# Kernel tuning notes

Hardware: AMD Instinct MI355X
Metric: run time of the kernel (lower is better)

## Reference

```python
import jax, jax.numpy as jnp
import numpy as np

N_NODES = 100000
N_EDGES = 1600000
N_GRAPHS = 512
IN_F, H1, H2 = 128, 128, 256
N_GROUPS, N_FAM = 16, 10


def setup_inputs() -> dict:
    key = jax.random.key(0)
    ks = jax.random.split(key, 8)
    x = jax.random.normal(ks[0], (N_NODES, IN_F), dtype=jnp.float32)
    edge_index = jax.random.randint(ks[1], (2, N_EDGES), 0, N_NODES, dtype=jnp.int64)
    batch = jnp.sort(jax.random.randint(ks[2], (N_NODES,), 0, N_GRAPHS, dtype=jnp.int64))
    W1 = jax.random.normal(ks[3], (IN_F, H1), dtype=jnp.float32) / np.sqrt(IN_F)
    b1 = jnp.zeros((H1,), dtype=jnp.float32)
    W2 = jax.random.normal(ks[4], (H1, H2), dtype=jnp.float32) / np.sqrt(H1)
    b2 = jnp.zeros((H2,), dtype=jnp.float32)
    Wg = jax.random.normal(ks[5], (H2, N_GROUPS), dtype=jnp.float32) / np.sqrt(H2)
    bg = jnp.zeros((N_GROUPS,), dtype=jnp.float32)
    Wf = jax.random.normal(ks[6], (N_GROUPS, H2, N_FAM), dtype=jnp.float32) / np.sqrt(H2)
    bf = jnp.zeros((N_GROUPS, N_FAM), dtype=jnp.float32)
    return {"x": x, "edge_index": edge_index, "batch": batch,
            "W1": W1, "b1": b1, "W2": W2, "b2": b2,
            "Wg": Wg, "bg": bg, "Wf": Wf, "bf": bf}


def gcn_conv(x, W, b, src, dst, num_nodes):
    # PyG GCNConv: add self-loops, symmetric normalization, scatter-add aggregation.
    xw = x @ W  # [N, out]
    deg = jax.ops.segment_sum(jnp.ones((src.shape[0],), x.dtype), dst,
                              num_segments=num_nodes) + 1.0  # +1 self-loop
    dinv = jax.lax.rsqrt(deg)
    coef = dinv[src] * dinv[dst]            # [E]
    msg = xw[src] * coef[:, None]           # gather + scale (memory-bound)
    agg = jax.ops.segment_sum(msg, dst, num_segments=num_nodes)
    agg = agg + xw * (dinv * dinv)[:, None]  # self-loop contribution
    return agg + b


def reference(x, edge_index, batch, W1, b1, W2, b2, Wg, bg, Wf, bf):
    src, dst = edge_index[0], edge_index[1]
    h = jax.nn.relu(gcn_conv(x, W1, b1, src, dst, N_NODES))
    # dropout p=0.5 is identity in eval mode
    h = gcn_conv(h, W2, b2, src, dst, N_NODES)
    # global mean pool over graphs
    sums = jax.ops.segment_sum(h, batch, num_segments=N_GRAPHS)       # [G, H2]
    cnts = jax.ops.segment_sum(jnp.ones((N_NODES,), h.dtype), batch,
                               num_segments=N_GRAPHS)
    pooled = sums / jnp.maximum(cnts, 1.0)[:, None]
    group_logits = pooled @ Wg + bg                                   # [G, num_groups]
    family_logits = jnp.einsum('bd,gdf->gbf', pooled, Wf) + bf[:, None, :]
    return group_logits, family_logits
```

## Files before the change

### kernel.cpp

```cpp
#include <hip/hip_runtime.h>

#define NN 100000
#define NE 1600000
#define NGR 512
#define KF 128
#define H2F 256
#define NGRP 16
#define NFAM 10

#define CH 128
#define NCHUNK ((NN + CH - 1) / CH)
#define PT 6656
#define NT ((NE + PT - 1) / PT)
#define PREPB_BLKS 64

typedef __attribute__((ext_vector_type(8))) short short8;
typedef __attribute__((ext_vector_type(4))) float floatx4;
typedef __attribute__((ext_vector_type(2))) float floatx2;
typedef __attribute__((ext_vector_type(2))) unsigned uintx2;

__device__ __forceinline__ unsigned short f2bf(float f) {
  unsigned u = __float_as_uint(f);
  unsigned r = (u + 0x7fff + ((u >> 16) & 1)) >> 16;
  return (unsigned short)r;
}
__device__ __forceinline__ float2 bf2f(unsigned u) {
  float2 r;
  r.x = __uint_as_float(u << 16);
  r.y = __uint_as_float(u & 0xffff0000u);
  return r;
}
__device__ __forceinline__ unsigned short pk_fp8(float a, float b) {
  return (unsigned short)__builtin_amdgcn_cvt_pk_fp8_f32(a, b, 0, false);
}
__device__ __forceinline__ floatx2 unpk_fp8(unsigned short u) {
  return __builtin_amdgcn_cvt_pk_f32_fp8((int)u, false);
}


__global__ __launch_bounds__(256) void k_histprep(const int* __restrict__ ei,
                                                  int* __restrict__ tot,
                                                  const float* __restrict__ W,
                                                  unsigned short* __restrict__ Bp) {
  __shared__ int lh[NCHUNK];
  int tid = threadIdx.x;
  if (blockIdx.x >= NT) {
    int idx = (blockIdx.x - NT) * 256 + tid;
    int j = idx & 7;
    int l = (idx >> 3) & 63;
    int rest = idx >> 9;
    int nc = rest & 7;
    int kc = rest >> 3;
    int k = kc * 32 + (l >> 4) * 8 + j;
    int nn = nc * 16 + (l & 15);
    Bp[idx] = f2bf(W[k * KF + nn]);
    return;
  }
  for (int g = tid; g < NCHUNK; g += 256) lh[g] = 0;
  __syncthreads();
  int base = blockIdx.x * PT;
  int nv = min(PT, NE - base);
  for (int i = tid; i < nv; i += 256) atomicAdd(&lh[ei[NE + base + i] >> 7], 1);
  __syncthreads();
  for (int g = tid; g < NCHUNK; g += 256) {
    int v = lh[g];
    if (v) atomicAdd(&tot[g], v);
  }
}


__global__ __launch_bounds__(256) void k_scantot(const int* __restrict__ tot,
                                                 int* __restrict__ cbase,
                                                 int* __restrict__ cursor) {
  __shared__ int ssc[256];
  int tid = threadIdx.x;
  int v4[4]; int loc = 0;
#pragma unroll
  for (int j = 0; j < 4; ++j) {
    int idx = tid * 4 + j;
    v4[j] = (idx < NCHUNK) ? tot[idx] : 0;
    loc += v4[j];
  }
  ssc[tid] = loc;
  __syncthreads();
  for (int off = 1; off < 256; off <<= 1) {
    int val = (tid >= off) ? ssc[tid - off] : 0;
    __syncthreads();
    ssc[tid] += val;
    __syncthreads();
  }
  int excl = ssc[tid] - loc;
#pragma unroll
  for (int j = 0; j < 4; ++j) {
    int idx = tid * 4 + j;
    if (idx < NCHUNK) { cbase[idx] = excl; cursor[idx] = excl; }
    excl += v4[j];
  }
  if (tid == 255) cbase[NCHUNK] = excl;
}


__global__ __launch_bounds__(256) void k_pscatter(const int* __restrict__ ei,
                                                  int* __restrict__ cursor,
                                                  int2* __restrict__ erec) {
  __shared__ int2 stage[PT];
  __shared__ int lstart[NCHUNK];
  __shared__ int lrun[NCHUNK];
  __shared__ int gbase[NCHUNK];
  __shared__ int ssc[256];
  int t0 = blockIdx.x, tid = threadIdx.x;
  for (int g = tid; g < NCHUNK; g += 256) lrun[g] = 0;
  __syncthreads();
  int base = t0 * PT;
  int nv = min(PT, NE - base);
  for (int i = tid; i < nv; i += 256) atomicAdd(&lrun[ei[NE + base + i] >> 7], 1);
  __syncthreads();
  int v4[4]; int loc = 0;
#pragma unroll
  for (int j = 0; j < 4; ++j) {
    int idx = tid * 4 + j;
    v4[j] = (idx < NCHUNK) ? lrun[idx] : 0;
    loc += v4[j];
  }
  ssc[tid] = loc;
  __syncthreads();
  for (int off = 1; off < 256; off <<= 1) {
    int val = (tid >= off) ? ssc[tid - off] : 0;
    __syncthreads();
    ssc[tid] += val;
    __syncthreads();
  }
  int excl = ssc[tid] - loc;
#pragma unroll
  for (int j = 0; j < 4; ++j) {
    int idx = tid * 4 + j;
    if (idx < NCHUNK) lstart[idx] = excl;
    excl += v4[j];
  }
  __syncthreads();
  for (int g = tid; g < NCHUNK; g += 256) {
    int cnt = ((g + 1 < NCHUNK) ? lstart[g + 1] : nv) - lstart[g];
    gbase[g] = cnt ? atomicAdd(&cursor[g], cnt) : 0;
    lrun[g] = lstart[g];
  }
  __syncthreads();
  for (int i = tid; i < nv; i += 256) {
    int s = ei[base + i], d = ei[NE + base + i];
    int pos = atomicAdd(&lrun[d >> 7], 1);
    stage[pos] = make_int2(s, d);
  }
  __syncthreads();
  for (int j = tid; j < nv; j += 256) {
    int2 r = stage[j];
    int g = r.y >> 7;
    erec[gbase[g] + (j - lstart[g])] = r;
  }
}


__global__ __launch_bounds__(256) void k_sort(const int2* __restrict__ erec,
                                              const int* __restrict__ cbase,
                                              int* __restrict__ esrc,
                                              float* __restrict__ ew,
                                              int* __restrict__ rowptr,
                                              float* __restrict__ dinv) {
  __shared__ int hist[CH];
  __shared__ int lrun[CH];
  __shared__ float ldv[CH];
  __shared__ int sc[256];
  const int c = blockIdx.x, tid = threadIdx.x;
  const int e0 = cbase[c], e1 = cbase[c + 1];
  const int nv = e1 - e0;
  if (tid < CH) hist[tid] = 0;
  __syncthreads();
  for (int i = tid; i < nv; i += 256) atomicAdd(&hist[erec[e0 + i].y & (CH - 1)], 1);
  __syncthreads();
  int deg = (tid < CH) ? hist[tid] : 0;
  sc[tid] = deg;
  __syncthreads();
  for (int off = 1; off < 256; off <<= 1) {
    int val = (tid >= off) ? sc[tid - off] : 0;
    __syncthreads();
    sc[tid] += val;
    __syncthreads();
  }
  int excl = sc[tid] - deg;
  int node = c * CH + tid;
  if (tid < CH) {
    lrun[tid] = excl;
    if (node < NN) {
      float dv = rsqrtf((float)(deg + 1));
      rowptr[node] = e0 + excl;
      dinv[node] = dv;
      ldv[tid] = dv;
    } else if (node == NN) {
      rowptr[NN] = e0 + excl;
    }
  }
  __syncthreads();
  for (int i = tid; i < nv; i += 256) {
    int2 r = erec[e0 + i];
    int ln = r.y & (CH - 1);
    int pos = atomicAdd(&lrun[ln], 1);
    esrc[e0 + pos] = r.x;
    ew[e0 + pos] = ldv[ln];
  }
}


__global__ __launch_bounds__(256) void k_gemm_mfma(const float* __restrict__ A,
                                                   const unsigned short* __restrict__ Bp,
                                                   const float* __restrict__ dinv,
                                                   unsigned short* __restrict__ C) {
  constexpr int K = 128;
  constexpr int NCH = KF / 16;
  const int wv = blockIdx.x * 4 + (threadIdx.x >> 6);
  const int row0 = wv * 16;
  if (row0 >= NN) return;
  const int lane = threadIdx.x & 63;
  const int m = lane & 15;
  const int q = lane >> 4;

  floatx4 acc[NCH];
#pragma unroll
  for (int i = 0; i < NCH; ++i) acc[i] = (floatx4){0.f, 0.f, 0.f, 0.f};

  const int arow = row0 + m;
#pragma unroll
  for (int kc = 0; kc < 4; ++kc) {
    const float* ap = A + (size_t)arow * K + kc * 32 + q * 8;
    float4 f0 = *(const float4*)ap;
    float4 f1 = *(const float4*)(ap + 4);
    short8 af;
    af[0] = (short)f2bf(f0.x); af[1] = (short)f2bf(f0.y);
    af[2] = (short)f2bf(f0.z); af[3] = (short)f2bf(f0.w);
    af[4] = (short)f2bf(f1.x); af[5] = (short)f2bf(f1.y);
    af[6] = (short)f2bf(f1.z); af[7] = (short)f2bf(f1.w);
    const unsigned short* bp = Bp + (size_t)kc * NCH * 512;
#pragma unroll
    for (int nc = 0; nc < NCH; ++nc) {
      short8 bfr = *(const short8*)(bp + (size_t)nc * 512 + lane * 8);
      acc[nc] = __builtin_amdgcn_mfma_f32_16x16x32_bf16(af, bfr, acc[nc], 0, 0, 0);
    }
  }

  float ds[4];
#pragma unroll
  for (int r = 0; r < 4; ++r) ds[r] = dinv[row0 + q * 4 + r];
#pragma unroll
  for (int nc = 0; nc < 4; ++nc) {
#pragma unroll
    for (int r = 0; r < 4; ++r) {
      int row = row0 + q * 4 + r;
      C[(size_t)row * 64 + nc * 16 + m] =
          pk_fp8(acc[nc][r] * ds[r], acc[nc + 4][r] * ds[r]);
    }
  }
}


__global__ __launch_bounds__(128) void k_agg1(const unsigned short* __restrict__ p,
                                              const float* __restrict__ bias,
                                              const int* __restrict__ rowptr,
                                              const int* __restrict__ esrc,
                                              const float* __restrict__ dinv,
                                              unsigned short* __restrict__ outp) {
  const int n = blockIdx.x * 2 + (threadIdx.x >> 6);
  const int t = threadIdx.x & 63;
  const int u = t & 31;
  const int half = t >> 5;
  const unsigned* __restrict__ prow = (const unsigned*)p;

  float a0 = 0.f, a1 = 0.f, a2 = 0.f, a3 = 0.f;

  if (half == 0) {
    unsigned v = prow[((unsigned)n << 5) + u];
    floatx2 lo = unpk_fp8((unsigned short)(v & 0xffffu));
    floatx2 hi = unpk_fp8((unsigned short)(v >> 16));
    a0 = lo.x; a1 = lo.y; a2 = hi.x; a3 = hi.y;
  }

  const int r0 = rowptr[n];
  const int r1 = rowptr[n + 1];
  int i = r0;

#define PAIR_TIER(NP)                                                  \
  for (; i + 2 * (NP) <= r1; i += 2 * (NP)) {                          \
    const int ib = i + half;                                           \
    unsigned s[NP];                                                    \
    _Pragma("unroll") for (int j = 0; j < (NP); ++j)                   \
        s[j] = (unsigned)esrc[ib + 2 * j];                             \
    unsigned v[NP];                                                    \
    _Pragma("unroll") for (int j = 0; j < (NP); ++j)                   \
        v[j] = prow[(s[j] << 5) + u];                                  \
    _Pragma("unroll") for (int j = 0; j < (NP); ++j) {                 \
      floatx2 lo = unpk_fp8((unsigned short)(v[j] & 0xffffu));         \
      floatx2 hi = unpk_fp8((unsigned short)(v[j] >> 16));             \
      a0 += lo.x; a1 += lo.y; a2 += hi.x; a3 += hi.y;                  \
    }                                                                  \
  }

  PAIR_TIER(8)
  PAIR_TIER(4)
  PAIR_TIER(2)
  PAIR_TIER(1)
#undef PAIR_TIER

  if (i < r1 && half == 0) {
    unsigned s = (unsigned)esrc[i];
    unsigned v = prow[(s << 5) + u];
    floatx2 lo = unpk_fp8((unsigned short)(v & 0xffffu));
    floatx2 hi = unpk_fp8((unsigned short)(v >> 16));
    a0 += lo.x; a1 += lo.y; a2 += hi.x; a3 += hi.y;
  }

  a0 += __shfl_down(a0, 32, 64);
  a1 += __shfl_down(a1, 32, 64);
  a2 += __shfl_down(a2, 32, 64);
  a3 += __shfl_down(a3, 32, 64);

  if (half == 0) {
    const float dn = dinv[n];
    float2 blo = *(const float2*)(bias + 2 * u);
    float2 bhi = *(const float2*)(bias + 64 + 2 * u);
    float x0 = fmaxf(fmaf(dn, a0, blo.x), 0.f) * dn;
    float x1 = fmaxf(fmaf(dn, a1, bhi.x), 0.f) * dn;
    float x2 = fmaxf(fmaf(dn, a2, blo.y), 0.f) * dn;
    float x3 = fmaxf(fmaf(dn, a3, bhi.y), 0.f) * dn;
    unsigned lo = pk_fp8(x0, x1);
    unsigned hi = pk_fp8(x2, x3);
    ((unsigned*)outp)[((unsigned)n << 5) + u] = lo | (hi << 16);
  }
}


__global__ __launch_bounds__(512) void k_aggpool(const unsigned short* __restrict__ p,
                                                 const int* __restrict__ batch,
                                                 const int* __restrict__ rowptr,
                                                 const int* __restrict__ esrc,
                                                 const float* __restrict__ ew,
                                                 const float* __restrict__ dinv,
                                                 const float* __restrict__ W2,
                                                 const float* __restrict__ b2,
                                                 const float* __restrict__ Wg,
                                                 const float* __restrict__ bg,
                                                 const float* __restrict__ Wf,
                                                 const float* __restrict__ bfb,
                                                 float* __restrict__ out) {
  __shared__ float sacc[8][128];
  __shared__ float pr[KF];
  __shared__ float pp[H2F];
  __shared__ int bnd[2];
  const int g = blockIdx.x;
  const int tid = threadIdx.x;
  if (tid < 2) {
    int target = g + tid;
    int lo = 0, hi = NN;
    while (lo < hi) { int mid = (lo + hi) >> 1; if (batch[mid] < target) lo = mid + 1; else hi = mid; }
    bnd[tid] = lo;
  }
  __syncthreads();
  const int start = bnd[0], end = bnd[1];
  const int wv = tid >> 6, t = tid & 63, u = t & 31, half = t >> 5;
  const unsigned* __restrict__ prow = (const unsigned*)p;

  float a0 = 0.f, a1 = 0.f, a2 = 0.f, a3 = 0.f;

  const int e0 = rowptr[start];
  const int e1 = rowptr[end];

#define EDGE_STEP(idx)                                                 \
  {                                                                    \
    unsigned s_ = (unsigned)esrc[(idx)];                               \
    float w_ = ew[(idx)];                                              \
    unsigned v_ = prow[(s_ << 5) + u];                                 \
    floatx2 lo = unpk_fp8((unsigned short)(v_ & 0xffffu));             \
    floatx2 hi = unpk_fp8((unsigned short)(v_ >> 16));                 \
    a0 = fmaf(w_, lo.x, a0); a1 = fmaf(w_, lo.y, a1);                  \
    a2 = fmaf(w_, hi.x, a2); a3 = fmaf(w_, hi.y, a3);                  \
  }

  int i = e0 + wv * 2 + half;
  for (; i + 48 < e1; i += 64) {
    int i0 = i, i1 = i + 16, i2 = i + 32, i3 = i + 48;
    unsigned s0 = (unsigned)esrc[i0], s1 = (unsigned)esrc[i1];
    unsigned s2 = (unsigned)esrc[i2], s3 = (unsigned)esrc[i3];
    float w0 = ew[i0], w1 = ew[i1], w2 = ew[i2], w3 = ew[i3];
    unsigned v0 = prow[(s0 << 5) + u];
    unsigned v1 = prow[(s1 << 5) + u];
    unsigned v2 = prow[(s2 << 5) + u];
    unsigned v3 = prow[(s3 << 5) + u];
    floatx2 f;
    f = unpk_fp8((unsigned short)(v0 & 0xffffu)); a0 = fmaf(w0, f.x, a0); a1 = fmaf(w0, f.y, a1);
    f = unpk_fp8((unsigned short)(v0 >> 16));     a2 = fmaf(w0, f.x, a2); a3 = fmaf(w0, f.y, a3);
    f = unpk_fp8((unsigned short)(v1 & 0xffffu)); a0 = fmaf(w1, f.x, a0); a1 = fmaf(w1, f.y, a1);
    f = unpk_fp8((unsigned short)(v1 >> 16));     a2 = fmaf(w1, f.x, a2); a3 = fmaf(w1, f.y, a3);
    f = unpk_fp8((unsigned short)(v2 & 0xffffu)); a0 = fmaf(w2, f.x, a0); a1 = fmaf(w2, f.y, a1);
    f = unpk_fp8((unsigned short)(v2 >> 16));     a2 = fmaf(w2, f.x, a2); a3 = fmaf(w2, f.y, a3);
    f = unpk_fp8((unsigned short)(v3 & 0xffffu)); a0 = fmaf(w3, f.x, a0); a1 = fmaf(w3, f.y, a1);
    f = unpk_fp8((unsigned short)(v3 >> 16));     a2 = fmaf(w3, f.x, a2); a3 = fmaf(w3, f.y, a3);
  }
  for (; i < e1; i += 16) EDGE_STEP(i)
#undef EDGE_STEP

  for (int n = start + wv * 2 + half; n < end; n += 16) {
    float w_ = dinv[n];
    unsigned v_ = prow[((unsigned)n << 5) + u];
    floatx2 lo = unpk_fp8((unsigned short)(v_ & 0xffffu));
    floatx2 hi = unpk_fp8((unsigned short)(v_ >> 16));
    a0 = fmaf(w_, lo.x, a0); a1 = fmaf(w_, lo.y, a1);
    a2 = fmaf(w_, hi.x, a2); a3 = fmaf(w_, hi.y, a3);
  }

  a0 += __shfl_down(a0, 32, 64);
  a1 += __shfl_down(a1, 32, 64);
  a2 += __shfl_down(a2, 32, 64);
  a3 += __shfl_down(a3, 32, 64);
  if (half == 0) {
    sacc[wv][2 * u] = a0;
    sacc[wv][2 * u + 1] = a2;
    sacc[wv][2 * u + 64] = a1;
    sacc[wv][2 * u + 65] = a3;
  }
  __syncthreads();
  if (tid < KF) {
    float v = 0.f;
#pragma unroll
    for (int w = 0; w < 8; ++w) v += sacc[w][tid];
    float c = fmaxf((float)(end - start), 1.f);
    pr[tid] = v / c;
  }
  __syncthreads();
  if (tid < H2F) {
    float acc = b2[tid];
#pragma unroll 8
    for (int d = 0; d < KF; ++d) acc = fmaf(pr[d], W2[d * H2F + tid], acc);
    pp[tid] = acc;
  }
  __syncthreads();
  if (tid < NGRP) {
    float a = bg[tid];
    for (int d = 0; d < H2F; ++d) a = fmaf(pp[d], Wg[d * NGRP + tid], a);
    out[g * NGRP + tid] = a;
  } else if (tid >= 64 && tid < 64 + NGRP * NFAM) {
    int uu = tid - 64;
    int gg = uu / NFAM;
    int ff = uu % NFAM;
    float a = bfb[gg * NFAM + ff];
    for (int d = 0; d < H2F; ++d) a = fmaf(pp[d], Wf[(gg * H2F + d) * NFAM + ff], a);
    out[NGR * NGRP + (size_t)gg * NGR * NFAM + g * NFAM + ff] = a;
  }
}


extern "C" void kernel_launch(void* const* d_in, const int* in_sizes, int n_in,
                              void* d_out, int out_size, void* d_ws, size_t ws_size,
                              hipStream_t stream) {
  const float* x    = (const float*)d_in[0];
  const int*   ei   = (const int*)d_in[1];
  const int*   batch= (const int*)d_in[2];
  const float* W1   = (const float*)d_in[3];
  const float* b1   = (const float*)d_in[4];
  const float* W2   = (const float*)d_in[5];
  const float* b2   = (const float*)d_in[6];
  const float* Wg   = (const float*)d_in[7];
  const float* bg   = (const float*)d_in[8];
  const float* Wf   = (const float*)d_in[9];
  const float* bfb  = (const float*)d_in[10];
  float* out = (float*)d_out;

  char* w = (char*)d_ws;
  auto take = [&](size_t bytes) {
    char* p = w;
    w += (bytes + 255) & ~(size_t)255;
    return (void*)p;
  };
  int*   tot   = (int*)take((size_t)NCHUNK * 4);
  int*   cbase = (int*)take((size_t)(NCHUNK + 1) * 4);
  int*   cursor= (int*)take((size_t)NCHUNK * 4);
  int2*  erec  = (int2*)take((size_t)NE * 8);
  int*   esrc  = (int*)take((size_t)NE * 4);
  float* ew    = (float*)take((size_t)NE * 4);
  int*   rowptr= (int*)take((size_t)(NN + 1) * 4);
  float* dinv  = (float*)take((size_t)NN * 4);
  unsigned short* Bp1 = (unsigned short*)take((size_t)KF * KF * 2);
  unsigned short* xw1 = (unsigned short*)take((size_t)NN * 64 * 2);
  unsigned short* h1  = (unsigned short*)take((size_t)NN * 64 * 2);

  hipMemsetAsync(tot, 0, (size_t)NCHUNK * 4, stream);
  k_histprep<<<NT + PREPB_BLKS, 256, 0, stream>>>(ei, tot, W1, Bp1);
  k_scantot<<<1, 256, 0, stream>>>(tot, cbase, cursor);
  k_pscatter<<<NT, 256, 0, stream>>>(ei, cursor, erec);
  k_sort<<<NCHUNK, 256, 0, stream>>>(erec, cbase, esrc, ew, rowptr, dinv);

  k_gemm_mfma<<<1563, 256, 0, stream>>>(x, Bp1, dinv, xw1);

  k_agg1<<<NN / 2, 128, 0, stream>>>(xw1, b1, rowptr, esrc, dinv, h1);
  k_aggpool<<<NGR, 512, 0, stream>>>(h1, batch, rowptr, esrc, ew, dinv,
                                     W2, b2, Wg, bg, Wf, bfb, out);
}
```

Before: 301.1 us.

## Split per-graph pooled aggregation across blocks with atomic partial sums

The fused aggregate-and-pool kernel, which ran one 512-thread block per graph, becomes a partial aggregation kernel. It launches NSPLIT 256-thread blocks per graph, each covering a slice of the graph's edges and nodes, and atomically adds its partial sums into a zeroed pooled buffer. A separate heads kernel then divides by node count and applies the W2, group and family projections. The aim is better GPU occupancy, since 512 large blocks underfill the device. The cost is an extra launch, float atomics that make summation order nondeterministic, and a larger memset.

```diff
diff --git a/kernel.cpp b/kernel.cpp
--- a/kernel.cpp
+++ b/kernel.cpp
@@ -14,21 +14,16 @@
 #define NT ((NE + PT - 1) / PT)
 #define PREPB_BLKS 64
 
+#define NSPLIT 8
+
 typedef __attribute__((ext_vector_type(8))) short short8;
 typedef __attribute__((ext_vector_type(4))) float floatx4;
 typedef __attribute__((ext_vector_type(2))) float floatx2;
-typedef __attribute__((ext_vector_type(2))) unsigned uintx2;
 
 __device__ __forceinline__ unsigned short f2bf(float f) {
   unsigned u = __float_as_uint(f);
   unsigned r = (u + 0x7fff + ((u >> 16) & 1)) >> 16;
   return (unsigned short)r;
-}
-__device__ __forceinline__ float2 bf2f(unsigned u) {
-  float2 r;
-  r.x = __uint_as_float(u << 16);
-  r.y = __uint_as_float(u & 0xffff0000u);
-  return r;
 }
 __device__ __forceinline__ unsigned short pk_fp8(float a, float b) {
   return (unsigned short)__builtin_amdgcn_cvt_pk_fp8_f32(a, b, 0, false);
@@ -334,24 +329,17 @@
 }
 
 
-__global__ __launch_bounds__(512) void k_aggpool(const unsigned short* __restrict__ p,
+__global__ __launch_bounds__(256) void k_aggpart(const unsigned short* __restrict__ p,
                                                  const int* __restrict__ batch,
                                                  const int* __restrict__ rowptr,
                                                  const int* __restrict__ esrc,
                                                  const float* __restrict__ ew,
                                                  const float* __restrict__ dinv,
-                                                 const float* __restrict__ W2,
-                                                 const float* __restrict__ b2,
-                                                 const float* __restrict__ Wg,
-                                                 const float* __restrict__ bg,
-                                                 const float* __restrict__ Wf,
-                                                 const float* __restrict__ bfb,
-                                                 float* __restrict__ out) {
-  __shared__ float sacc[8][128];
-  __shared__ float pr[KF];
-  __shared__ float pp[H2F];
+                                                 float* __restrict__ pooled) {
+  __shared__ float sacc[4][128];
   __shared__ int bnd[2];
-  const int g = blockIdx.x;
+  const int g = blockIdx.x / NSPLIT;
+  const int part = blockIdx.x % NSPLIT;
   const int tid = threadIdx.x;
   if (tid < 2) {
     int target = g + tid;
@@ -368,6 +356,10 @@
 
   const int e0 = rowptr[start];
   const int e1 = rowptr[end];
+  const int elen = e1 - e0;
+  const int eper = (elen + NSPLIT - 1) / NSPLIT;
+  const int is = min(e0 + part * eper, e1);
+  const int ie = min(is + eper, e1);
 
 #define EDGE_STEP(idx)                                                 \
   {                                                                    \
@@ -380,9 +372,9 @@
     a2 = fmaf(w_, hi.x, a2); a3 = fmaf(w_, hi.y, a3);                  \
   }
 
-  int i = e0 + wv * 2 + half;
-  for (; i + 48 < e1; i += 64) {
-    int i0 = i, i1 = i + 16, i2 = i + 32, i3 = i + 48;
+  int i = is + wv * 2 + half;
+  for (; i + 24 < ie; i += 32) {
+    int i0 = i, i1 = i + 8, i2 = i + 16, i3 = i + 24;
     unsigned s0 = (unsigned)esrc[i0], s1 = (unsigned)esrc[i1];
     unsigned s2 = (unsigned)esrc[i2], s3 = (unsigned)esrc[i3];
     float w0 = ew[i0], w1 = ew[i1], w2 = ew[i2], w3 = ew[i3];
@@ -400,10 +392,14 @@
     f = unpk_fp8((unsigned short)(v3 & 0xffffu)); a0 = fmaf(w3, f.x, a0); a1 = fmaf(w3, f.y, a1);
     f = unpk_fp8((unsigned short)(v3 >> 16));     a2 = fmaf(w3, f.x, a2); a3 = fmaf(w3, f.y, a3);
   }
-  for (; i < e1; i += 16) EDGE_STEP(i)
+  for (; i < ie; i += 8) EDGE_STEP(i)
 #undef EDGE_STEP
 
-  for (int n = start + wv * 2 + half; n < end; n += 16) {
+  const int nlen = end - start;
+  const int nper = (nlen + NSPLIT - 1) / NSPLIT;
+  const int ns = min(start + part * nper, end);
+  const int ne = min(ns + nper, end);
+  for (int n = ns + wv * 2 + half; n < ne; n += 8) {
     float w_ = dinv[n];
     unsigned v_ = prow[((unsigned)n << 5) + u];
     floatx2 lo = unpk_fp8((unsigned short)(v_ & 0xffffu));
@@ -424,19 +420,42 @@
   }
   __syncthreads();
   if (tid < KF) {
-    float v = 0.f;
-#pragma unroll
-    for (int w = 0; w < 8; ++w) v += sacc[w][tid];
-    float c = fmaxf((float)(end - start), 1.f);
-    pr[tid] = v / c;
-  }
-  __syncthreads();
-  if (tid < H2F) {
-    float acc = b2[tid];
+    float v = sacc[0][tid] + sacc[1][tid] + sacc[2][tid] + sacc[3][tid];
+    atomicAdd(&pooled[(size_t)g * KF + tid], v);
+  }
+}
+
+
+__global__ __launch_bounds__(256) void k_heads(const float* __restrict__ pooled,
+                                               const int* __restrict__ batch,
+                                               const float* __restrict__ W2,
+                                               const float* __restrict__ b2,
+                                               const float* __restrict__ Wg,
+                                               const float* __restrict__ bg,
+                                               const float* __restrict__ Wf,
+                                               const float* __restrict__ bfb,
+                                               float* __restrict__ out) {
+  __shared__ float pr[KF];
+  __shared__ float pp[H2F];
+  __shared__ int bnd[2];
+  const int g = blockIdx.x;
+  const int tid = threadIdx.x;
+  if (tid < 2) {
+    int target = g + tid;
+    int lo = 0, hi = NN;
+    while (lo < hi) { int mid = (lo + hi) >> 1; if (batch[mid] < target) lo = mid + 1; else hi = mid; }
+    bnd[tid] = lo;
+  }
+  __syncthreads();
+  if (tid < KF) {
+    float c = fmaxf((float)(bnd[1] - bnd[0]), 1.f);
+    pr[tid] = pooled[(size_t)g * KF + tid] / c;
+  }
+  __syncthreads();
+  float acc = b2[tid];
 #pragma unroll 8
-    for (int d = 0; d < KF; ++d) acc = fmaf(pr[d], W2[d * H2F + tid], acc);
-    pp[tid] = acc;
-  }
+  for (int d = 0; d < KF; ++d) acc = fmaf(pr[d], W2[d * H2F + tid], acc);
+  pp[tid] = acc;
   __syncthreads();
   if (tid < NGRP) {
     float a = bg[tid];
@@ -476,6 +495,7 @@
     return (void*)p;
   };
   int*   tot   = (int*)take((size_t)NCHUNK * 4);
+  float* pooled= (float*)take((size_t)NGR * KF * 4);
   int*   cbase = (int*)take((size_t)(NCHUNK + 1) * 4);
   int*   cursor= (int*)take((size_t)NCHUNK * 4);
   int2*  erec  = (int2*)take((size_t)NE * 8);
@@ -487,7 +507,9 @@
   unsigned short* xw1 = (unsigned short*)take((size_t)NN * 64 * 2);
   unsigned short* h1  = (unsigned short*)take((size_t)NN * 64 * 2);
 
-  hipMemsetAsync(tot, 0, (size_t)NCHUNK * 4, stream);
+  size_t zbytes = (size_t)((char*)pooled - (char*)tot) + (size_t)NGR * KF * 4;
+  hipMemsetAsync(tot, 0, zbytes, stream);
+
   k_histprep<<<NT + PREPB_BLKS, 256, 0, stream>>>(ei, tot, W1, Bp1);
   k_scantot<<<1, 256, 0, stream>>>(tot, cbase, cursor);
   k_pscatter<<<NT, 256, 0, stream>>>(ei, cursor, erec);
@@ -496,6 +518,6 @@
   k_gemm_mfma<<<1563, 256, 0, stream>>>(x, Bp1, dinv, xw1);
 
   k_agg1<<<NN / 2, 128, 0, stream>>>(xw1, b1, rowptr, esrc, dinv, h1);
-  k_aggpool<<<NGR, 512, 0, stream>>>(h1, batch, rowptr, esrc, ew, dinv,
-                                     W2, b2, Wg, bg, Wf, bfb, out);
-}
+  k_aggpart<<<NGR * NSPLIT, 256, 0, stream>>>(h1, batch, rowptr, esrc, ew, dinv, pooled);
+  k_heads<<<NGR, 256, 0, stream>>>(pooled, batch, W2, b2, Wg, bg, Wf, bfb, out);
+}
```

New measurement: 297.0 us. Within noise of the previous version (-1.4%).
